# Optimization experiments

Measured on AMD Instinct MI355X. Metric: run time of the kernel, lower is better.

Reference implementation:

```python
import jax, jax.numpy as jnp
import numpy as np

SIZE = 640
FPN_STRIDES = (8, 16, 32, 64, 128)
REG_MAX = 16
NUM_CLASSES = 80
TOPK = 45


def _build_anchors():
    pts, boxes, strides = [], [], []
    for s in FPN_STRIDES:
        h, w = SIZE // s, SIZE // s
        y, x = np.meshgrid(np.arange(h), np.arange(w), indexing='ij')
        yf = y.ravel().astype(np.float32)
        xf = x.ravel().astype(np.float32)
        pts.append(np.stack([(yf + 0.5) * s, (xf + 0.5) * s], -1))
        boxes.append(np.stack([yf * s, xf * s, (yf + 1) * s, (xf + 1) * s], -1))
        strides.append(np.full(h * w, s, np.float32))
    return (jnp.asarray(np.concatenate(pts), jnp.float32),
            jnp.asarray(np.concatenate(boxes), jnp.float32),
            jnp.asarray(np.concatenate(strides), jnp.float32))


ANCHOR_PTS, ANCHOR_BOXES, STRIDES = _build_anchors()
NUM_ANCHORS = ANCHOR_PTS.shape[0]  # 8525


def _iou(b1, b2):
    # elementwise IoU over trailing dim 4 in (y1, x1, y2, x2); axes are symmetric
    ty = jnp.maximum(b1[..., 0], b2[..., 0])
    tx = jnp.maximum(b1[..., 1], b2[..., 1])
    by = jnp.minimum(b1[..., 2], b2[..., 2])
    bx = jnp.minimum(b1[..., 3], b2[..., 3])
    inter = jnp.clip(by - ty, 0.0) * jnp.clip(bx - tx, 0.0)
    a1 = (b1[..., 2] - b1[..., 0]) * (b1[..., 3] - b1[..., 1])
    a2 = (b2[..., 2] - b2[..., 0]) * (b2[..., 3] - b2[..., 1])
    return inter / (a1 + a2 - inter)


def _assign_single(gt_cls, gt_bbox, pred_d):
    # gt_cls: (N,), gt_bbox: (N,4), pred_d: (4,A)
    A, N, C = NUM_ANCHORS, gt_bbox.shape[0], NUM_CLASSES
    pts, boxes, strides = ANCHOR_PTS, ANCHOR_BOXES, STRIDES
    centers = (gt_bbox[:, :2] + gt_bbox[:, 2:]) / 2
    dist = jnp.linalg.norm(centers[:, None, :] - pts[None, :, :], axis=-1)  # (N,A)
    _, k_ind = jax.lax.top_k(-dist, TOPK)  # (N,K) nearest anchors
    kb = boxes[k_ind]  # (N,K,4)
    Dg = _iou(gt_bbox[:, None, :], kb)  # (N,K)
    tg = Dg.mean(1) + Dg.std(1, ddof=1)  # torch .std() is unbiased
    ap = pts[k_ind]  # (N,K,2)
    inside = ((gt_bbox[:, None, 0] <= ap[..., 0]) & (ap[..., 0] <= gt_bbox[:, None, 2]) &
              (gt_bbox[:, None, 1] <= ap[..., 1]) & (ap[..., 1] <= gt_bbox[:, None, 3]))
    valid = (Dg >= tg[:, None]) & inside  # (N,K)
    n_idx = jnp.broadcast_to(jnp.arange(N, dtype=jnp.int32)[:, None], (N, TOPK))
    pri = jnp.where(valid, n_idx, -1).ravel()
    a_flat = k_ind.ravel()
    win_d = jnp.full((A,), -1, jnp.int32).at[a_flat].max(pri)
    wb = gt_bbox[jnp.clip(win_d, 0)]  # (A,4)
    gt_d = jnp.stack([(pts[:, 0] - wb[:, 0]) / strides,
                      (pts[:, 1] - wb[:, 1]) / strides,
                      (wb[:, 2] - pts[:, 0]) / strides,
                      (wb[:, 3] - pts[:, 1]) / strides], 0)  # (4,A) = [dtop,dleft,dbottom,dright]
    gt_dfl = jnp.where(win_d[None, :] >= 0, gt_d, jnp.inf)
    cls_pair = gt_cls.astype(jnp.int32)[n_idx]  # (N,K)
    ca = (cls_pair * A + k_ind).ravel()
    win_q = jnp.full((C * A,), -1, jnp.int32).at[ca].max(pri).reshape(C, A)
    gbq = gt_bbox[jnp.clip(win_q, 0)]  # (C,A,4)
    # _overlap_tlbr: decode(gt_d)*stride around anchor point, clamped -> clipped gt box
    box1 = jnp.clip(gbq, 0.0, float(SIZE))  # (C,A,4)
    rd = pred_d * strides[None, :]  # (4,A) raw offsets
    box2 = jnp.stack([jnp.clip(pts[:, 0] - rd[0], 0.0, float(SIZE)),
                      jnp.clip(pts[:, 1] - rd[1], 0.0, float(SIZE)),
                      jnp.clip(pts[:, 0] + rd[2], 0.0, float(SIZE)),
                      jnp.clip(pts[:, 1] + rd[3], 0.0, float(SIZE))], -1)  # (A,4)
    q = _iou(box1, box2[None, :, :])  # (C,A)
    gt_qfl = jnp.where(win_q >= 0, q, 0.0)
    return gt_qfl, gt_dfl


def setup_inputs() -> dict:
    key = jax.random.key(0)
    k1, k2, k3, k4 = jax.random.split(key, 4)
    B, N = 16, 64
    tl = jax.random.uniform(k1, (B, N, 2), jnp.float32, 0.0, SIZE - 64.0)
    wh = jax.random.uniform(k2, (B, N, 2), jnp.float32, 16.0, 256.0)
    br = jnp.minimum(tl + wh, float(SIZE))
    gt_bboxes = jnp.concatenate([tl, br], -1)  # (y1,x1,y2,x2)
    gt_clses = jax.random.randint(k3, (B, N), 0, NUM_CLASSES)
    pred_reg = jax.random.normal(k4, (B, 4, REG_MAX + 1, NUM_ANCHORS), jnp.float32)
    return {"gt_clses_batch": gt_clses, "gt_bboxes_batch": gt_bboxes,
            "pred_reg_batch": pred_reg}


def reference(gt_clses_batch, gt_bboxes_batch, pred_reg_batch):
    p = jax.nn.softmax(pred_reg_batch, axis=2)
    rng = jnp.arange(REG_MAX + 1, dtype=p.dtype).reshape(1, 1, -1, 1)
    pred_d = (p * rng).sum(2)  # (B,4,A) integral distribution -> expected offsets
    qfl, dfl = jax.vmap(_assign_single)(gt_clses_batch, gt_bboxes_batch, pred_d)
    return qfl, dfl, ANCHOR_PTS, STRIDES
```

## Files before the change

### kernel.cpp

```cpp
#include <hip/hip_runtime.h>
#include <math.h>
#include <float.h>

#define A_TOTAL 8525
#define NUM_B   16
#define NUM_N   64
#define NUM_C   80
#define K_TOP   45
#define SIZE_F  640.0f

#define UNASSIGNED_SENTINEL 1.0e30f

#define CUTOFF_KEY 0x43000000u
#define NBINS_PAD  2304
#define CAND_MAX   768

#define QFL_FLOATS  ((size_t)NUM_B * NUM_C * A_TOTAL)
#define MASK_WORDS  (NUM_B * A_TOTAL)
#define MASK_VEC4   ((MASK_WORDS * 2) / 4)

__device__ __forceinline__ void anchor_decode(int a, float& py, float& px, float& s,
                                              float& qy0, float& qx0, float& qy1, float& qx1) {
    int rel, w; float sf;
    if (a < 6400)      { rel = a;        w = 80; sf = 8.f;   }
    else if (a < 8000) { rel = a - 6400; w = 40; sf = 16.f;  }
    else if (a < 8400) { rel = a - 8000; w = 20; sf = 32.f;  }
    else if (a < 8500) { rel = a - 8400; w = 10; sf = 64.f;  }
    else               { rel = a - 8500; w = 5;  sf = 128.f; }
    int y = rel / w, x = rel - y * w;
    float yf = (float)y, xf = (float)x;
    py  = (yf + 0.5f) * sf;  px  = (xf + 0.5f) * sf;
    qy0 = yf * sf;           qx0 = xf * sf;
    qy1 = (yf + 1.f) * sf;   qx1 = (xf + 1.f) * sf;
    s = sf;
}

__device__ __forceinline__ unsigned int dist_key_yx(int yy, int xx, float s,
                                                    float cy, float cx) {
    float py = __fmul_rn(__fadd_rn((float)yy, 0.5f), s);
    float px = __fmul_rn(__fadd_rn((float)xx, 0.5f), s);
    float dy = __fadd_rn(cy, -py);
    float dx = __fadd_rn(cx, -px);
    float v = sqrtf(__fadd_rn(__fmul_rn(dy, dy), __fmul_rn(dx, dx)));
    return __float_as_uint(v);
}

__device__ __forceinline__ float iou_box(float ay0, float ax0, float ay1, float ax1,
                                         float by0, float bx0, float by1, float bx1) {
    float ty = fmaxf(ay0, by0), tx = fmaxf(ax0, bx0);
    float by = fminf(ay1, by1), bx = fminf(ax1, bx1);
    float ih = fmaxf(__fadd_rn(by, -ty), 0.f);
    float iw = fmaxf(__fadd_rn(bx, -tx), 0.f);
    float inter = __fmul_rn(ih, iw);
    float a1 = __fmul_rn(__fadd_rn(ay1, -ay0), __fadd_rn(ax1, -ax0));
    float a2 = __fmul_rn(__fadd_rn(by1, -by0), __fadd_rn(bx1, -bx0));
    return inter / __fadd_rn(__fadd_rn(a1, a2), -inter);
}

__global__ __launch_bounds__(256) void prep_kernel(unsigned long long* __restrict__ mask,
                                                   float* __restrict__ opts,
                                                   float* __restrict__ ostr) {
    size_t gid = (size_t)blockIdx.x * 256 + threadIdx.x;
    size_t nthreads = (size_t)gridDim.x * 256;

    uint4* m4 = (uint4*)mask;
    for (size_t i = gid; i < MASK_VEC4; i += nthreads)
        m4[i] = make_uint4(0u, 0u, 0u, 0u);

    for (size_t a = gid; a < A_TOTAL; a += nthreads) {
        float py, px, s, q0, q1, q2, q3;
        anchor_decode((int)a, py, px, s, q0, q1, q2, q3);
        opts[2 * a]     = py;
        opts[2 * a + 1] = px;
        ostr[a]         = s;
    }
}

__global__ __launch_bounds__(256) void assign_kernel(const float* __restrict__ gt_bbox,
                                                     unsigned long long* __restrict__ mask) {
    __shared__ unsigned int hist[NBINS_PAD];
    __shared__ unsigned int wtot[4];
    __shared__ unsigned int cand_key[CAND_MAX];
    __shared__ int          cand_idx[CAND_MAX];
    __shared__ int          s_candn;
    __shared__ int          s_B;
    __shared__ int          sel[K_TOP];
    __shared__ float        dg[K_TOP];
    __shared__ float        s_tg;

    const int   LH[5] = {80, 40, 20, 10, 5};
    const int   LB[5] = {0, 6400, 8000, 8400, 8500};
    const float LS[5] = {8.f, 16.f, 32.f, 64.f, 128.f};

    int tid = threadIdx.x;
    int lane = tid & 63, wid = tid >> 6;
    int b = blockIdx.x >> 6;
    int n = blockIdx.x & 63;
    const float* gb = gt_bbox + (size_t)(b * NUM_N + n) * 4;
    float g0 = gb[0], g1 = gb[1], g2 = gb[2], g3 = gb[3];
    float cy = __fmul_rn(__fadd_rn(g0, g2), 0.5f);
    float cx = __fmul_rn(__fadd_rn(g1, g3), 0.5f);

    int wy0[5], wx0[5], wnc[5], wcl[5];
#pragma unroll
    for (int l = 0; l < 5; ++l) {
        float s = LS[l]; int H = LH[l];
        int y0 = (int)((cy - 68.f) / s) - 1; if (y0 < 0) y0 = 0;
        int y1 = (int)((cy + 68.f) / s) + 1; if (y1 > H - 1) y1 = H - 1;
        int x0 = (int)((cx - 68.f) / s) - 1; if (x0 < 0) x0 = 0;
        int x1 = (int)((cx + 68.f) / s) + 1; if (x1 > H - 1) x1 = H - 1;
        wy0[l] = y0; wx0[l] = x0;
        wnc[l] = x1 - x0 + 1;
        wcl[l] = (y1 - y0 + 1) * wnc[l];
    }

    for (int i = tid; i < NBINS_PAD; i += 256) hist[i] = 0u;
    if (tid == 0) s_candn = 0;
    __syncthreads();

#pragma unroll
    for (int l = 0; l < 5; ++l) {
        int nc = wnc[l], cells = wcl[l];
        for (int t = tid; t < cells; t += 256) {
            int r = t / nc, c = t - r * nc;
            unsigned int key = dist_key_yx(wy0[l] + r, wx0[l] + c, LS[l], cy, cx);
            if (key < CUTOFF_KEY) atomicAdd(&hist[key >> 19], 1u);
        }
    }
    __syncthreads();

    unsigned int psum = 0;
    int base = tid * 9;
#pragma unroll
    for (int k = 0; k < 9; ++k) psum += hist[base + k];
    unsigned int x = psum;
    for (int off = 1; off < 64; off <<= 1) {
        unsigned int y = __shfl_up(x, off, 64);
        if (lane >= off) x += y;
    }
    if (lane == 63) wtot[wid] = x;
    __syncthreads();
    unsigned int wbase = 0;
    for (int w = 0; w < 4; ++w) wbase += (w < wid) ? wtot[w] : 0u;
    unsigned int inc = wbase + x;
    unsigned int exc = inc - psum;
    if (exc < (unsigned)K_TOP && inc >= (unsigned)K_TOP) {
        unsigned int cum = exc;
        int bbin = base;
        while (cum + hist[bbin] < (unsigned)K_TOP) { cum += hist[bbin]; ++bbin; }
        s_B = bbin;
    }
    __syncthreads();

    int B = s_B;
#pragma unroll
    for (int l = 0; l < 5; ++l) {
        int nc = wnc[l], cells = wcl[l];
        for (int t = tid; t < cells; t += 256) {
            int r = t / nc, c = t - r * nc;
            int yy = wy0[l] + r, xx = wx0[l] + c;
            unsigned int key = dist_key_yx(yy, xx, LS[l], cy, cx);
            if (key < CUTOFF_KEY && (int)(key >> 19) <= B) {
                int pos = atomicAdd(&s_candn, 1);
                if (pos < CAND_MAX) {
                    cand_key[pos] = key;
                    cand_idx[pos] = LB[l] + yy * LH[l] + xx;
                }
            }
        }
    }
    __syncthreads();

    int M = s_candn < CAND_MAX ? s_candn : CAND_MAX;
    for (int i = tid; i < M; i += 256) {
        unsigned int ki = cand_key[i]; int ii = cand_idx[i];
        int rank = 0;
        for (int j = 0; j < M; ++j) {
            unsigned int kj = cand_key[j]; int ij = cand_idx[j];
            rank += (kj < ki || (kj == ki && ij < ii)) ? 1 : 0;
        }
        if (rank < K_TOP) sel[rank] = ii;
    }
    __syncthreads();

    if (tid < K_TOP) {
        int a = sel[tid];
        float py, px, s, q0, q1, q2, q3;
        anchor_decode(a, py, px, s, q0, q1, q2, q3);
        dg[tid] = iou_box(g0, g1, g2, g3, q0, q1, q2, q3);
    }
    __syncthreads();
    if (tid == 0) {
        float sum = 0.f;
        for (int k = 0; k < K_TOP; ++k) sum = __fadd_rn(sum, dg[k]);
        float mean = sum / (float)K_TOP;
        float ss = 0.f;
        for (int k = 0; k < K_TOP; ++k) {
            float d = __fadd_rn(dg[k], -mean);
            ss = __fadd_rn(ss, __fmul_rn(d, d));
        }
        s_tg = __fadd_rn(mean, sqrtf(ss / (float)(K_TOP - 1)));
    }
    __syncthreads();
    if (tid < K_TOP) {
        int a = sel[tid];
        float py, px, s, q0, q1, q2, q3;
        anchor_decode(a, py, px, s, q0, q1, q2, q3);
        bool inside = (g0 <= py) && (py <= g2) && (g1 <= px) && (px <= g3);
        if (inside && dg[tid] >= s_tg) {
            atomicOr(&mask[(size_t)b * A_TOTAL + a], 1ull << n);
        }
    }
}

__global__ __launch_bounds__(256) void output_kernel(const int* __restrict__ gt_cls,
                                                     const float* __restrict__ gt_bbox,
                                                     const float* __restrict__ pred_reg,
                                                     const unsigned long long* __restrict__ mask,
                                                     float* __restrict__ qfl,
                                                     float* __restrict__ dfl) {
    __shared__ float s_gb[NUM_N * 4];
    __shared__ float s_gc[NUM_N * 4];
    __shared__ int   s_cls[NUM_N];

    int tid = threadIdx.x;
    int b = blockIdx.y;
    if (tid < NUM_N * 4) {
        float v = gt_bbox[(size_t)b * NUM_N * 4 + tid];
        s_gb[tid] = v;
        s_gc[tid] = fminf(fmaxf(v, 0.f), SIZE_F);
    }
    if (tid < NUM_N) s_cls[tid] = gt_cls[b * NUM_N + tid];
    __syncthreads();

    int a = blockIdx.x * 256 + tid;
    if (a >= A_TOTAL) return;

    unsigned long long m64 = mask[(size_t)b * A_TOTAL + a];
    float* dflp = dfl + (size_t)b * 4 * A_TOTAL + a;
    float* qflp = qfl + (size_t)b * NUM_C * A_TOTAL + a;

#pragma unroll
    for (int c = 0; c < NUM_C; ++c) qflp[(size_t)c * A_TOTAL] = 0.f;

    if (m64 == 0ull) {
        dflp[0]           = UNASSIGNED_SENTINEL;
        dflp[A_TOTAL]     = UNASSIGNED_SENTINEL;
        dflp[2 * A_TOTAL] = UNASSIGNED_SENTINEL;
        dflp[3 * A_TOTAL] = UNASSIGNED_SENTINEL;
        return;
    }

    float py, px, s, q0, q1, q2, q3;
    anchor_decode(a, py, px, s, q0, q1, q2, q3);

    float rd[4];
    const float* pr = pred_reg + (size_t)b * 4 * 17 * A_TOTAL + a;
#pragma unroll
    for (int d = 0; d < 4; ++d) {
        float xv[17];
#pragma unroll
        for (int j = 0; j < 17; ++j) xv[j] = pr[(size_t)(d * 17 + j) * A_TOTAL];
        float m = xv[0];
#pragma unroll
        for (int j = 1; j < 17; ++j) m = fmaxf(m, xv[j]);
        float S = 0.f, dot = 0.f;
#pragma unroll
        for (int j = 0; j < 17; ++j) {
            float t = __expf(xv[j] - m);
            S += t;
            dot += t * (float)j;
        }
        rd[d] = (dot / S) * s;
    }
    float b2y0 = fminf(fmaxf(py - rd[0], 0.f), SIZE_F);
    float b2x0 = fminf(fmaxf(px - rd[1], 0.f), SIZE_F);
    float b2y1 = fminf(fmaxf(py + rd[2], 0.f), SIZE_F);
    float b2x1 = fminf(fmaxf(px + rd[3], 0.f), SIZE_F);

    {
        int n = 63 - __clzll(m64);
        dflp[0]            = (py - s_gb[n * 4 + 0]) / s;
        dflp[A_TOTAL]      = (px - s_gb[n * 4 + 1]) / s;
        dflp[2 * A_TOTAL]  = (s_gb[n * 4 + 2] - py) / s;
        dflp[3 * A_TOTAL]  = (s_gb[n * 4 + 3] - px) / s;
    }

    unsigned long long seen0 = 0ull, seen1 = 0ull;
    unsigned long long mm = m64;
    while (mm) {
        int n = 63 - __clzll(mm);
        mm &= ~(1ull << n);
        int c = s_cls[n];
        bool done;
        if (c < 64) {
            unsigned long long bit = 1ull << c;
            done = (seen0 & bit) != 0ull; seen0 |= bit;
        } else {
            unsigned long long bit = 1ull << (c - 64);
            done = (seen1 & bit) != 0ull; seen1 |= bit;
        }
        if (!done) {
            qflp[(size_t)c * A_TOTAL] = iou_box(s_gc[n * 4 + 0], s_gc[n * 4 + 1],
                                                s_gc[n * 4 + 2], s_gc[n * 4 + 3],
                                                b2y0, b2x0, b2y1, b2x1);
        }
    }
}

extern "C" void kernel_launch(void* const* d_in, const int* in_sizes, int n_in,
                              void* d_out, int out_size, void* d_ws, size_t ws_size,
                              hipStream_t stream) {
    const int*   gt_cls   = (const int*)d_in[0];
    const float* gt_bbox  = (const float*)d_in[1];
    const float* pred_reg = (const float*)d_in[2];

    float* qfl  = (float*)d_out;
    float* dfl  = qfl + QFL_FLOATS;
    float* opts = dfl + (size_t)NUM_B * 4 * A_TOTAL;
    float* ostr = opts + (size_t)A_TOTAL * 2;

    unsigned long long* mask = (unsigned long long*)d_ws;

    hipLaunchKernelGGL(prep_kernel, dim3(256), dim3(256), 0, stream, mask, opts, ostr);
    hipLaunchKernelGGL(assign_kernel, dim3(NUM_B * NUM_N), dim3(256), 0, stream, gt_bbox, mask);
    hipLaunchKernelGGL(output_kernel, dim3((A_TOTAL + 255) / 256, NUM_B), dim3(256), 0, stream,
                       gt_cls, gt_bbox, pred_reg, mask, qfl, dfl);
}
```

Baseline: 113.4 us.

## Move qfl zero-fill and dfl sentinel fill into prep kernel with wider grid

The default qfl zeros and dfl sentinels are now written by the prep kernel using 16-byte vector stores over a larger grid. Previously the output kernel did this with scalar strided stores after assignment. The output kernel now returns early for unassigned anchors and only writes entries that were assigned. This takes the bulk of the output writes off the critical path behind assign_kernel and vectorizes them, at the cost of writing some qfl/dfl locations twice.

```diff
diff --git a/kernel.cpp b/kernel.cpp
--- a/kernel.cpp
+++ b/kernel.cpp
@@ -16,8 +16,11 @@
 #define CAND_MAX   768
 
 #define QFL_FLOATS  ((size_t)NUM_B * NUM_C * A_TOTAL)
+#define DFL_FLOATS  ((size_t)NUM_B * 4 * A_TOTAL)
 #define MASK_WORDS  (NUM_B * A_TOTAL)
 #define MASK_VEC4   ((MASK_WORDS * 2) / 4)
+#define QFL_VEC4    (QFL_FLOATS / 4)
+#define DFL_VEC4    (DFL_FLOATS / 4)
 
 __device__ __forceinline__ void anchor_decode(int a, float& py, float& px, float& s,
                                               float& qy0, float& qx0, float& qy1, float& qx1) {
@@ -58,14 +61,27 @@
 }
 
 __global__ __launch_bounds__(256) void prep_kernel(unsigned long long* __restrict__ mask,
+                                                   float* __restrict__ qfl,
+                                                   float* __restrict__ dfl,
                                                    float* __restrict__ opts,
                                                    float* __restrict__ ostr) {
     size_t gid = (size_t)blockIdx.x * 256 + threadIdx.x;
     size_t nthreads = (size_t)gridDim.x * 256;
 
+    const uint4 z4 = make_uint4(0u, 0u, 0u, 0u);
+    uint4* q4 = (uint4*)qfl;
+    for (size_t i = gid; i < QFL_VEC4; i += nthreads)
+        q4[i] = z4;
+
+    const unsigned int su = __float_as_uint(UNASSIGNED_SENTINEL);
+    const uint4 s4 = make_uint4(su, su, su, su);
+    uint4* d4 = (uint4*)dfl;
+    for (size_t i = gid; i < DFL_VEC4; i += nthreads)
+        d4[i] = s4;
+
     uint4* m4 = (uint4*)mask;
     for (size_t i = gid; i < MASK_VEC4; i += nthreads)
-        m4[i] = make_uint4(0u, 0u, 0u, 0u);
+        m4[i] = z4;
 
     for (size_t a = gid; a < A_TOTAL; a += nthreads) {
         float py, px, s, q0, q1, q2, q3;
@@ -237,19 +253,10 @@
     if (a >= A_TOTAL) return;
 
     unsigned long long m64 = mask[(size_t)b * A_TOTAL + a];
+    if (m64 == 0ull) return;
+
     float* dflp = dfl + (size_t)b * 4 * A_TOTAL + a;
     float* qflp = qfl + (size_t)b * NUM_C * A_TOTAL + a;
-
-#pragma unroll
-    for (int c = 0; c < NUM_C; ++c) qflp[(size_t)c * A_TOTAL] = 0.f;
-
-    if (m64 == 0ull) {
-        dflp[0]           = UNASSIGNED_SENTINEL;
-        dflp[A_TOTAL]     = UNASSIGNED_SENTINEL;
-        dflp[2 * A_TOTAL] = UNASSIGNED_SENTINEL;
-        dflp[3 * A_TOTAL] = UNASSIGNED_SENTINEL;
-        return;
-    }
 
     float py, px, s, q0, q1, q2, q3;
     anchor_decode(a, py, px, s, q0, q1, q2, q3);
@@ -317,12 +324,13 @@
 
     float* qfl  = (float*)d_out;
     float* dfl  = qfl + QFL_FLOATS;
-    float* opts = dfl + (size_t)NUM_B * 4 * A_TOTAL;
+    float* opts = dfl + DFL_FLOATS;
     float* ostr = opts + (size_t)A_TOTAL * 2;
 
     unsigned long long* mask = (unsigned long long*)d_ws;
 
-    hipLaunchKernelGGL(prep_kernel, dim3(256), dim3(256), 0, stream, mask, opts, ostr);
+    hipLaunchKernelGGL(prep_kernel, dim3(2048), dim3(256), 0, stream,
+                       mask, qfl, dfl, opts, ostr);
     hipLaunchKernelGGL(assign_kernel, dim3(NUM_B * NUM_N), dim3(256), 0, stream, gt_bbox, mask);
     hipLaunchKernelGGL(output_kernel, dim3((A_TOTAL + 255) / 256, NUM_B), dim3(256), 0, stream,
                        gt_cls, gt_bbox, pred_reg, mask, qfl, dfl);
```

Result: no change. 112.0 us (-1.2%).

## Replace global anchor bitmask with per-GT compact lists and drop prep kernel

Applied to the files above, without the earlier changes.

The assign kernel now writes a compact list of positive anchor indices for each GT into workspace instead of doing atomicOr into a zeroed global 64-bit mask. Each output block rebuilds its local mask in shared memory by scanning all 64 lists for its batch. This removes the prep kernel launch, the mask zeroing pass and the global atomics. Anchor points and strides are now written by the b==0 blocks of the output kernel. The cost is that every output block reads the 64 list counts and entries serially, which adds latency at the start of each block.

```diff
diff --git a/kernel.cpp b/kernel.cpp
--- a/kernel.cpp
+++ b/kernel.cpp
@@ -16,8 +16,9 @@
 #define CAND_MAX   768
 
 #define QFL_FLOATS  ((size_t)NUM_B * NUM_C * A_TOTAL)
-#define MASK_WORDS  (NUM_B * A_TOTAL)
-#define MASK_VEC4   ((MASK_WORDS * 2) / 4)
+#define DFL_FLOATS  ((size_t)NUM_B * 4 * A_TOTAL)
+
+#define LIST_STRIDE 64
 
 __device__ __forceinline__ void anchor_decode(int a, float& py, float& px, float& s,
                                               float& qy0, float& qx0, float& qy1, float& qx1) {
@@ -57,32 +58,14 @@
     return inter / __fadd_rn(__fadd_rn(a1, a2), -inter);
 }
 
-__global__ __launch_bounds__(256) void prep_kernel(unsigned long long* __restrict__ mask,
-                                                   float* __restrict__ opts,
-                                                   float* __restrict__ ostr) {
-    size_t gid = (size_t)blockIdx.x * 256 + threadIdx.x;
-    size_t nthreads = (size_t)gridDim.x * 256;
-
-    uint4* m4 = (uint4*)mask;
-    for (size_t i = gid; i < MASK_VEC4; i += nthreads)
-        m4[i] = make_uint4(0u, 0u, 0u, 0u);
-
-    for (size_t a = gid; a < A_TOTAL; a += nthreads) {
-        float py, px, s, q0, q1, q2, q3;
-        anchor_decode((int)a, py, px, s, q0, q1, q2, q3);
-        opts[2 * a]     = py;
-        opts[2 * a + 1] = px;
-        ostr[a]         = s;
-    }
-}
-
 __global__ __launch_bounds__(256) void assign_kernel(const float* __restrict__ gt_bbox,
-                                                     unsigned long long* __restrict__ mask) {
+                                                     int* __restrict__ lists) {
     __shared__ unsigned int hist[NBINS_PAD];
     __shared__ unsigned int wtot[4];
     __shared__ unsigned int cand_key[CAND_MAX];
     __shared__ int          cand_idx[CAND_MAX];
     __shared__ int          s_candn;
+    __shared__ int          s_outn;
     __shared__ int          s_B;
     __shared__ int          sel[K_TOP];
     __shared__ float        dg[K_TOP];
@@ -96,6 +79,7 @@
     int lane = tid & 63, wid = tid >> 6;
     int b = blockIdx.x >> 6;
     int n = blockIdx.x & 63;
+    int* mylist = lists + (size_t)(b * NUM_N + n) * LIST_STRIDE;
     const float* gb = gt_bbox + (size_t)(b * NUM_N + n) * 4;
     float g0 = gb[0], g1 = gb[1], g2 = gb[2], g3 = gb[3];
     float cy = __fmul_rn(__fadd_rn(g0, g2), 0.5f);
@@ -115,7 +99,7 @@
     }
 
     for (int i = tid; i < NBINS_PAD; i += 256) hist[i] = 0u;
-    if (tid == 0) s_candn = 0;
+    if (tid == 0) { s_candn = 0; s_outn = 0; }
     __syncthreads();
 
 #pragma unroll
@@ -208,35 +192,70 @@
         anchor_decode(a, py, px, s, q0, q1, q2, q3);
         bool inside = (g0 <= py) && (py <= g2) && (g1 <= px) && (px <= g3);
         if (inside && dg[tid] >= s_tg) {
-            atomicOr(&mask[(size_t)b * A_TOTAL + a], 1ull << n);
-        }
-    }
+            int pos = atomicAdd(&s_outn, 1);
+            mylist[1 + pos] = a;
+        }
+    }
+    __syncthreads();
+    if (tid == 0) mylist[0] = s_outn;
 }
 
 __global__ __launch_bounds__(256) void output_kernel(const int* __restrict__ gt_cls,
                                                      const float* __restrict__ gt_bbox,
                                                      const float* __restrict__ pred_reg,
-                                                     const unsigned long long* __restrict__ mask,
+                                                     const int* __restrict__ lists,
                                                      float* __restrict__ qfl,
-                                                     float* __restrict__ dfl) {
-    __shared__ float s_gb[NUM_N * 4];
-    __shared__ float s_gc[NUM_N * 4];
-    __shared__ int   s_cls[NUM_N];
+                                                     float* __restrict__ dfl,
+                                                     float* __restrict__ opts,
+                                                     float* __restrict__ ostr) {
+    __shared__ float        s_gb[NUM_N * 4];
+    __shared__ float        s_gc[NUM_N * 4];
+    __shared__ int          s_cls[NUM_N];
+    __shared__ unsigned int s_mlo[256];
+    __shared__ unsigned int s_mhi[256];
 
     int tid = threadIdx.x;
     int b = blockIdx.y;
+    int a0 = blockIdx.x * 256;
+
     if (tid < NUM_N * 4) {
         float v = gt_bbox[(size_t)b * NUM_N * 4 + tid];
         s_gb[tid] = v;
         s_gc[tid] = fminf(fmaxf(v, 0.f), SIZE_F);
     }
     if (tid < NUM_N) s_cls[tid] = gt_cls[b * NUM_N + tid];
-    __syncthreads();
-
-    int a = blockIdx.x * 256 + tid;
+    s_mlo[tid] = 0u;
+    s_mhi[tid] = 0u;
+    __syncthreads();
+
+    for (int n = 0; n < NUM_N; ++n) {
+        const int* L = lists + (size_t)(b * NUM_N + n) * LIST_STRIDE;
+        int cnt = L[0];
+        for (int i = tid; i < cnt; i += 256) {
+            int rel = L[1 + i] - a0;
+            if (0 <= rel && rel < 256) {
+                if (n < 32) atomicOr(&s_mlo[rel], 1u << n);
+                else        atomicOr(&s_mhi[rel], 1u << (n - 32));
+            }
+        }
+    }
+    __syncthreads();
+
+    int a = a0 + tid;
     if (a >= A_TOTAL) return;
 
-    unsigned long long m64 = mask[(size_t)b * A_TOTAL + a];
+    unsigned long long m64 =
+        ((unsigned long long)s_mhi[tid] << 32) | (unsigned long long)s_mlo[tid];
+
+    float py, px, s, q0, q1, q2, q3;
+    anchor_decode(a, py, px, s, q0, q1, q2, q3);
+
+    if (b == 0) {
+        opts[2 * a]     = py;
+        opts[2 * a + 1] = px;
+        ostr[a]         = s;
+    }
+
     float* dflp = dfl + (size_t)b * 4 * A_TOTAL + a;
     float* qflp = qfl + (size_t)b * NUM_C * A_TOTAL + a;
 
@@ -250,9 +269,6 @@
         dflp[3 * A_TOTAL] = UNASSIGNED_SENTINEL;
         return;
     }
-
-    float py, px, s, q0, q1, q2, q3;
-    anchor_decode(a, py, px, s, q0, q1, q2, q3);
 
     float rd[4];
     const float* pr = pred_reg + (size_t)b * 4 * 17 * A_TOTAL + a;
@@ -317,13 +333,13 @@
 
     float* qfl  = (float*)d_out;
     float* dfl  = qfl + QFL_FLOATS;
-    float* opts = dfl + (size_t)NUM_B * 4 * A_TOTAL;
+    float* opts = dfl + DFL_FLOATS;
     float* ostr = opts + (size_t)A_TOTAL * 2;
 
-    unsigned long long* mask = (unsigned long long*)d_ws;
-
-    hipLaunchKernelGGL(prep_kernel, dim3(256), dim3(256), 0, stream, mask, opts, ostr);
-    hipLaunchKernelGGL(assign_kernel, dim3(NUM_B * NUM_N), dim3(256), 0, stream, gt_bbox, mask);
+    int* lists = (int*)d_ws;
+
+    hipLaunchKernelGGL(assign_kernel, dim3(NUM_B * NUM_N), dim3(256), 0, stream,
+                       gt_bbox, lists);
     hipLaunchKernelGGL(output_kernel, dim3((A_TOTAL + 255) / 256, NUM_B), dim3(256), 0, stream,
-                       gt_cls, gt_bbox, pred_reg, mask, qfl, dfl);
-}
+                       gt_cls, gt_bbox, pred_reg, lists, qfl, dfl, opts, ostr);
+}
```

Result: slower. 134.3 us (+18.5%).
